# Performance work log

Hardware: AMD Instinct MI355X
Metric: run time of the kernel (lower is better)

The kernel has to match this reference:

```python
import jax, jax.numpy as jnp
import numpy as np


def setup_inputs() -> dict:
    key = jax.random.key(0)
    k1, k2, k3, k4 = jax.random.split(key, 4)
    N, E, D, B = 50000, 100000, 64, 16
    atom_features = jax.random.normal(k1, (N, D), dtype=jnp.float32)
    bond_features = jax.random.normal(k2, (E, B), dtype=jnp.float32)
    pair_indices = jax.random.randint(k3, (E, 2), 0, N, dtype=jnp.int32)
    kernel = jax.random.normal(k4, (B, D * D), dtype=jnp.float32) * (1.0 / np.sqrt(B))
    bias = jnp.zeros((D * D,), dtype=jnp.float32)
    return {
        "atom_features": atom_features,
        "bond_features": bond_features,
        "pair_indices": pair_indices,
        "kernel": kernel,
        "bias": bias,
    }


def reference(atom_features, bond_features, pair_indices, kernel, bias):
    N, D = atom_features.shape
    # Per-edge transformation matrix: [E, D, D]
    edge_mat = (bond_features @ kernel + bias).reshape(-1, D, D)
    # Gather neighbor atom features: [E, D]
    neighbors = atom_features[pair_indices[:, 1]]
    # Per-edge matvec (matmul with expand/squeeze in original): [E, D]
    transformed = jnp.einsum("eij,ej->ei", edge_mat, neighbors)
    # Scatter-add into destination atoms: [N, D]
    aggregated = jax.ops.segment_sum(transformed, pair_indices[:, 0], num_segments=N)
    return aggregated
```

## Files before the change

kernel.cpp:

```cpp
#include <hip/hip_runtime.h>

typedef _Float16 half8  __attribute__((ext_vector_type(8)));
typedef _Float16 half2v __attribute__((ext_vector_type(2)));
typedef float    f32x4  __attribute__((ext_vector_type(4)));

#define BB 16
#define NB_B 17
#define BM 128
#define NT 8
#define PACK_BLKS 34
#define ZERO_BLKS 1024

__device__ __forceinline__ void gll16(const void* g, void* l) {
  __builtin_amdgcn_global_load_lds(
      (const __attribute__((address_space(1))) void*)g,
      (__attribute__((address_space(3))) void*)l, 16, 0, 0);
}

__global__ void prep(const float* __restrict__ kern, const float* __restrict__ bias,
                     _Float16* __restrict__ ktg, f32x4* __restrict__ out4, int n4) {
  if (blockIdx.x < PACK_BLKS) {
    int g = blockIdx.x * 256 + threadIdx.x;
    int s = g >> 8, t = (g >> 6) & 3, l = g & 63;
    int i = t * 16 + (l & 15);
    int k0 = s * 32 + (l >> 4) * 8;
    _Float16 v[8];
#pragma unroll
    for (int e = 0; e < 8; ++e) {
      int k = k0 + e, b = k >> 6, j = k & 63;
      float x = (b < BB) ? kern[b * 4096 + i * 64 + j] : bias[i * 64 + j];
      v[e] = (_Float16)x;
    }
    size_t dst = (size_t)(s >> 1) * 4096 + (size_t)(s & 1) * 2048 + t * 512 + l * 8;
    *(half8*)(ktg + dst) = *(const half8*)v;
  } else {
    int i = (blockIdx.x - PACK_BLKS) * 256 + threadIdx.x;
    for (; i < n4; i += ZERO_BLKS * 256) out4[i] = (f32x4){0.f, 0.f, 0.f, 0.f};
  }
}

__global__ __launch_bounds__(256, 4)
void edge_gemm(const float* __restrict__ atom, const float* __restrict__ bond,
               const int* __restrict__ pair, const _Float16* __restrict__ ktg,
               float* __restrict__ out, int E) {
  __shared__ __align__(16) _Float16 nb[BM * 64];
  __shared__ __align__(16) char bbuf[2][8192];
  __shared__ __align__(16) _Float16 bndh[NB_B * 16 * NT];
  __shared__ int srcs[BM];
  __shared__ int nbrs[BM];

  const int tid = threadIdx.x;
  const int e0  = blockIdx.x * BM;

  if (tid < BM) {
    const int e = e0 + tid;
    const bool valid = e < E;
    int2 p2 = valid ? *(const int2*)(pair + 2 * e) : (int2){0, 0};
    srcs[tid] = p2.x;
    nbrs[tid] = p2.y;
  }
  gll16((const char*)ktg + tid * 16,        (char*)bbuf[0] + tid * 16);
  gll16((const char*)ktg + 4096 + tid * 16, (char*)bbuf[0] + 4096 + tid * 16);
  __syncthreads();

  if (tid < BM) {
    const int e = e0 + tid;
    const bool valid = e < E;
    const int wl = tid & 15, wt = tid >> 4;
    const f32x4* brow = (const f32x4*)(bond + (size_t)e * BB);
#pragma unroll
    for (int q = 0; q < 4; ++q) {
      f32x4 bv = {0.f, 0.f, 0.f, 0.f};
      if (valid) bv = brow[q];
#pragma unroll
      for (int z = 0; z < 4; ++z)
        bndh[((q * 4 + z) * 16 + wl) * NT + wt] = (_Float16)bv[z];
    }
    bndh[(16 * 16 + wl) * NT + wt] = valid ? (_Float16)1.0f : (_Float16)0.0f;
  }

#pragma unroll
  for (int it = 0; it < 4; ++it) {
    const int idx = it * 256 + tid;
    const int r = idx >> 3, c8 = idx & 7;
    const int nbr = nbrs[r];
    const bool valid = (e0 + r) < E;
    f32x4 x0 = {0.f,0.f,0.f,0.f}, x1 = {0.f,0.f,0.f,0.f};
    if (valid) {
      const f32x4* arow = (const f32x4*)(atom + (size_t)nbr * 64);
      x0 = arow[2 * c8]; x1 = arow[2 * c8 + 1];
    }
    _Float16 h[8];
    h[0] = (_Float16)x0[0]; h[1] = (_Float16)x0[1]; h[2] = (_Float16)x0[2]; h[3] = (_Float16)x0[3];
    h[4] = (_Float16)x1[0]; h[5] = (_Float16)x1[1]; h[6] = (_Float16)x1[2]; h[7] = (_Float16)x1[3];
    *(half8*)((char*)nb + r * 128 + ((c8 ^ (r & 7)) << 4)) = *(const half8*)h;
  }
  __syncthreads();

  const int lane = tid & 63, wave = tid >> 6;
  const int l15 = lane & 15, lg = lane >> 4;

  half8 a[NT][2];
#pragma unroll
  for (int t = 0; t < NT; ++t) {
    const int r = t * 16 + l15;
    const int rb = r * 128, sw = (r & 7) << 4;
#pragma unroll
    for (int p = 0; p < 2; ++p)
      a[t][p] = *(const half8*)((const char*)nb + rb + (((p * 4 + lg) << 4) ^ sw));
  }

  f32x4 acc[NT];
#pragma unroll
  for (int t = 0; t < NT; ++t) acc[t] = (f32x4){0.f, 0.f, 0.f, 0.f};

  for (int b = 0; b < NB_B; ++b) {
    if (b + 1 < NB_B) {
      const char* src = (const char*)ktg + (size_t)(b + 1) * 8192;
      char* dst = (char*)bbuf[(b + 1) & 1];
      gll16(src + tid * 16,        dst + tid * 16);
      gll16(src + 4096 + tid * 16, dst + 4096 + tid * 16);
    }
    const half8 sv = *(const half8*)&bndh[(b * 16 + l15) * NT];
    const char* bp = (const char*)bbuf[b & 1] + wave * 1024 + lane * 16;
#pragma unroll
    for (int sp = 0; sp < 2; ++sp) {
      const half8 bf = *(const half8*)(bp + sp * 4096);
#pragma unroll
      for (int t = 0; t < NT; ++t) {
        const _Float16 s = sv[t];
        const half2v sc = {s, s};
        half8 as = a[t][sp];
        half2v* ap = (half2v*)&as;
#pragma unroll
        for (int q = 0; q < 4; ++q) ap[q] = ap[q] * sc;
        acc[t] = __builtin_amdgcn_mfma_f32_16x16x32_f16(as, bf, acc[t], 0, 0, 0);
      }
    }
    __syncthreads();
  }

#pragma unroll
  for (int t = 0; t < NT; ++t) {
#pragma unroll
    for (int rr = 0; rr < 4; ++rr) {
      const int el = t * 16 + lg * 4 + rr;
      if (e0 + el < E)
        atomicAdd(out + (size_t)srcs[el] * 64 + wave * 16 + l15, acc[t][rr]);
    }
  }
}

extern "C" void kernel_launch(void* const* d_in, const int* in_sizes, int n_in,
                              void* d_out, int out_size, void* d_ws, size_t ws_size,
                              hipStream_t stream) {
  const float* atom = (const float*)d_in[0];
  const float* bond = (const float*)d_in[1];
  const int*   pair = (const int*)d_in[2];
  const float* kern = (const float*)d_in[3];
  const float* bias = (const float*)d_in[4];
  float* out = (float*)d_out;
  _Float16* ktg = (_Float16*)d_ws;

  const int E  = in_sizes[1] / BB;
  const int n4 = out_size / 4;

  prep<<<PACK_BLKS + ZERO_BLKS, 256, 0, stream>>>(kern, bias, ktg, (f32x4*)out, n4);
  edge_gemm<<<(E + BM - 1) / BM, 256, 0, stream>>>(atom, bond, pair, ktg, out, E);
}
```

Before: 115.1 us.

## Load kernel tiles directly to registers with 2x2 wave tiling, drop LDS staging

```diff
diff --git a/kernel.cpp b/kernel.cpp
--- a/kernel.cpp
+++ b/kernel.cpp
@@ -1,6 +1,7 @@
 #include <hip/hip_runtime.h>
 
 typedef _Float16 half8  __attribute__((ext_vector_type(8)));
+typedef _Float16 half4v __attribute__((ext_vector_type(4)));
 typedef _Float16 half2v __attribute__((ext_vector_type(2)));
 typedef float    f32x4  __attribute__((ext_vector_type(4)));
 
@@ -10,12 +11,6 @@
 #define NT 8
 #define PACK_BLKS 34
 #define ZERO_BLKS 1024
-
-__device__ __forceinline__ void gll16(const void* g, void* l) {
-  __builtin_amdgcn_global_load_lds(
-      (const __attribute__((address_space(1))) void*)g,
-      (__attribute__((address_space(3))) void*)l, 16, 0, 0);
-}
 
 __global__ void prep(const float* __restrict__ kern, const float* __restrict__ bias,
                      _Float16* __restrict__ ktg, f32x4* __restrict__ out4, int n4) {
@@ -39,12 +34,11 @@
   }
 }
 
-__global__ __launch_bounds__(256, 4)
+__global__ __launch_bounds__(256, 3)
 void edge_gemm(const float* __restrict__ atom, const float* __restrict__ bond,
                const int* __restrict__ pair, const _Float16* __restrict__ ktg,
                float* __restrict__ out, int E) {
   __shared__ __align__(16) _Float16 nb[BM * 64];
-  __shared__ __align__(16) char bbuf[2][8192];
   __shared__ __align__(16) _Float16 bndh[NB_B * 16 * NT];
   __shared__ int srcs[BM];
   __shared__ int nbrs[BM];
@@ -59,8 +53,6 @@
     srcs[tid] = p2.x;
     nbrs[tid] = p2.y;
   }
-  gll16((const char*)ktg + tid * 16,        (char*)bbuf[0] + tid * 16);
-  gll16((const char*)ktg + 4096 + tid * 16, (char*)bbuf[0] + 4096 + tid * 16);
   __syncthreads();
 
   if (tid < BM) {
@@ -98,55 +90,69 @@
   __syncthreads();
 
   const int lane = tid & 63, wave = tid >> 6;
+  const int wm = wave >> 1, wn = wave & 1;
   const int l15 = lane & 15, lg = lane >> 4;
 
-  half8 a[NT][2];
+  half8 a[4][2];
 #pragma unroll
-  for (int t = 0; t < NT; ++t) {
-    const int r = t * 16 + l15;
+  for (int t = 0; t < 4; ++t) {
+    const int r = wm * 64 + t * 16 + l15;
     const int rb = r * 128, sw = (r & 7) << 4;
 #pragma unroll
     for (int p = 0; p < 2; ++p)
       a[t][p] = *(const half8*)((const char*)nb + rb + (((p * 4 + lg) << 4) ^ sw));
   }
 
-  f32x4 acc[NT];
+  f32x4 acc[4][2];
 #pragma unroll
-  for (int t = 0; t < NT; ++t) acc[t] = (f32x4){0.f, 0.f, 0.f, 0.f};
+  for (int t = 0; t < 4; ++t) {
+    acc[t][0] = (f32x4){0.f, 0.f, 0.f, 0.f};
+    acc[t][1] = (f32x4){0.f, 0.f, 0.f, 0.f};
+  }
 
-  for (int b = 0; b < NB_B; ++b) {
-    if (b + 1 < NB_B) {
-      const char* src = (const char*)ktg + (size_t)(b + 1) * 8192;
-      char* dst = (char*)bbuf[(b + 1) & 1];
-      gll16(src + tid * 16,        dst + tid * 16);
-      gll16(src + 4096 + tid * 16, dst + 4096 + tid * 16);
+  const _Float16* bp  = ktg + (size_t)wn * 1024 + (size_t)lane * 8;
+  const _Float16* scp = &bndh[l15 * NT + wm * 4];
+
+  half8 bf[3][4];
+#pragma unroll
+  for (int rr = 0; rr < 3; ++rr)
+#pragma unroll
+    for (int f = 0; f < 4; ++f)
+      bf[rr][f] = *(const half8*)(bp + rr * 4096 + (f >> 1) * 2048 + (f & 1) * 512);
+
+#pragma unroll
+  for (int r = 0; r < NB_B; ++r) {
+    const int slot = r % 3;
+    const half4v sv = *(const half4v*)(scp + r * 128);
+#pragma unroll
+    for (int t = 0; t < 4; ++t) {
+      const half2v sc = {sv[t], sv[t]};
+      half8 a0 = a[t][0], a1 = a[t][1];
+      half2v* a0p = (half2v*)&a0; half2v* a1p = (half2v*)&a1;
+#pragma unroll
+      for (int q = 0; q < 4; ++q) { a0p[q] = a0p[q] * sc; a1p[q] = a1p[q] * sc; }
+      acc[t][0] = __builtin_amdgcn_mfma_f32_16x16x32_f16(a0, bf[slot][0], acc[t][0], 0, 0, 0);
+      acc[t][1] = __builtin_amdgcn_mfma_f32_16x16x32_f16(a0, bf[slot][1], acc[t][1], 0, 0, 0);
+      acc[t][0] = __builtin_amdgcn_mfma_f32_16x16x32_f16(a1, bf[slot][2], acc[t][0], 0, 0, 0);
+      acc[t][1] = __builtin_amdgcn_mfma_f32_16x16x32_f16(a1, bf[slot][3], acc[t][1], 0, 0, 0);
     }
-    const half8 sv = *(const half8*)&bndh[(b * 16 + l15) * NT];
-    const char* bp = (const char*)bbuf[b & 1] + wave * 1024 + lane * 16;
+    if (r + 3 < NB_B) {
 #pragma unroll
-    for (int sp = 0; sp < 2; ++sp) {
-      const half8 bf = *(const half8*)(bp + sp * 4096);
-#pragma unroll
-      for (int t = 0; t < NT; ++t) {
-        const _Float16 s = sv[t];
-        const half2v sc = {s, s};
-        half8 as = a[t][sp];
-        half2v* ap = (half2v*)&as;
-#pragma unroll
-        for (int q = 0; q < 4; ++q) ap[q] = ap[q] * sc;
-        acc[t] = __builtin_amdgcn_mfma_f32_16x16x32_f16(as, bf, acc[t], 0, 0, 0);
-      }
+      for (int f = 0; f < 4; ++f)
+        bf[slot][f] = *(const half8*)(bp + (r + 3) * 4096 + (f >> 1) * 2048 + (f & 1) * 512);
     }
-    __syncthreads();
   }
 
 #pragma unroll
-  for (int t = 0; t < NT; ++t) {
+  for (int t = 0; t < 4; ++t) {
 #pragma unroll
     for (int rr = 0; rr < 4; ++rr) {
-      const int el = t * 16 + lg * 4 + rr;
-      if (e0 + el < E)
-        atomicAdd(out + (size_t)srcs[el] * 64 + wave * 16 + l15, acc[t][rr]);
+      const int el = wm * 64 + t * 16 + lg * 4 + rr;
+      if (e0 + el < E) {
+        float* dst = out + (size_t)srcs[el] * 64 + wn * 32 + l15;
+        atomicAdd(dst,      acc[t][0][rr]);
+        atomicAdd(dst + 16, acc[t][1][rr]);
+      }
     }
   }
 }
```

Result: faster. 110.9 us (-3.6%).

## Halve edge tile to 64 and use a 2x2 wave tiling of MFMA outputs

Applied to the files above, without the earlier changes.

```diff
diff --git a/kernel.cpp b/kernel.cpp
--- a/kernel.cpp
+++ b/kernel.cpp
@@ -6,8 +6,7 @@
 
 #define BB 16
 #define NB_B 17
-#define BM 128
-#define NT 8
+#define BM 64
 #define PACK_BLKS 34
 #define ZERO_BLKS 1024
 
@@ -39,13 +38,13 @@
   }
 }
 
-__global__ __launch_bounds__(256, 4)
+__global__ __launch_bounds__(256, 5)
 void edge_gemm(const float* __restrict__ atom, const float* __restrict__ bond,
                const int* __restrict__ pair, const _Float16* __restrict__ ktg,
                float* __restrict__ out, int E) {
   __shared__ __align__(16) _Float16 nb[BM * 64];
   __shared__ __align__(16) char bbuf[2][8192];
-  __shared__ __align__(16) _Float16 bndh[NB_B * 16 * NT];
+  __shared__ _Float16 bndh[NB_B * BM];
   __shared__ int srcs[BM];
   __shared__ int nbrs[BM];
 
@@ -66,21 +65,19 @@
   if (tid < BM) {
     const int e = e0 + tid;
     const bool valid = e < E;
-    const int wl = tid & 15, wt = tid >> 4;
     const f32x4* brow = (const f32x4*)(bond + (size_t)e * BB);
 #pragma unroll
     for (int q = 0; q < 4; ++q) {
       f32x4 bv = {0.f, 0.f, 0.f, 0.f};
       if (valid) bv = brow[q];
 #pragma unroll
-      for (int z = 0; z < 4; ++z)
-        bndh[((q * 4 + z) * 16 + wl) * NT + wt] = (_Float16)bv[z];
+      for (int z = 0; z < 4; ++z) bndh[(q * 4 + z) * BM + tid] = (_Float16)bv[z];
     }
-    bndh[(16 * 16 + wl) * NT + wt] = valid ? (_Float16)1.0f : (_Float16)0.0f;
+    bndh[16 * BM + tid] = valid ? (_Float16)1.0f : (_Float16)0.0f;
   }
 
 #pragma unroll
-  for (int it = 0; it < 4; ++it) {
+  for (int it = 0; it < 2; ++it) {
     const int idx = it * 256 + tid;
     const int r = idx >> 3, c8 = idx & 7;
     const int nbr = nbrs[r];
@@ -98,21 +95,24 @@
   __syncthreads();
 
   const int lane = tid & 63, wave = tid >> 6;
+  const int wm = wave >> 1, wn = wave & 1;
   const int l15 = lane & 15, lg = lane >> 4;
 
-  half8 a[NT][2];
+  half8 a[2][2];
 #pragma unroll
-  for (int t = 0; t < NT; ++t) {
-    const int r = t * 16 + l15;
+  for (int t = 0; t < 2; ++t) {
+    const int r = wm * 32 + t * 16 + l15;
     const int rb = r * 128, sw = (r & 7) << 4;
 #pragma unroll
     for (int p = 0; p < 2; ++p)
       a[t][p] = *(const half8*)((const char*)nb + rb + (((p * 4 + lg) << 4) ^ sw));
   }
 
-  f32x4 acc[NT];
+  f32x4 acc[2][2];
 #pragma unroll
-  for (int t = 0; t < NT; ++t) acc[t] = (f32x4){0.f, 0.f, 0.f, 0.f};
+  for (int t = 0; t < 2; ++t)
+#pragma unroll
+    for (int n = 0; n < 2; ++n) acc[t][n] = (f32x4){0.f, 0.f, 0.f, 0.f};
 
   for (int b = 0; b < NB_B; ++b) {
     if (b + 1 < NB_B) {
@@ -121,32 +121,36 @@
       gll16(src + tid * 16,        dst + tid * 16);
       gll16(src + 4096 + tid * 16, dst + 4096 + tid * 16);
     }
-    const half8 sv = *(const half8*)&bndh[(b * 16 + l15) * NT];
-    const char* bp = (const char*)bbuf[b & 1] + wave * 1024 + lane * 16;
+    const _Float16 s0 = bndh[b * BM + wm * 32 + l15];
+    const _Float16 s1 = bndh[b * BM + wm * 32 + 16 + l15];
+    const half2v sc0 = {s0, s0}, sc1 = {s1, s1};
+    const char* bp = (const char*)bbuf[b & 1] + (size_t)(wn * 2) * 1024 + lane * 16;
 #pragma unroll
     for (int sp = 0; sp < 2; ++sp) {
-      const half8 bf = *(const half8*)(bp + sp * 4096);
+      half8 a0 = a[0][sp], a1 = a[1][sp];
+      half2v* a0p = (half2v*)&a0; half2v* a1p = (half2v*)&a1;
 #pragma unroll
-      for (int t = 0; t < NT; ++t) {
-        const _Float16 s = sv[t];
-        const half2v sc = {s, s};
-        half8 as = a[t][sp];
-        half2v* ap = (half2v*)&as;
+      for (int q = 0; q < 4; ++q) { a0p[q] = a0p[q] * sc0; a1p[q] = a1p[q] * sc1; }
 #pragma unroll
-        for (int q = 0; q < 4; ++q) ap[q] = ap[q] * sc;
-        acc[t] = __builtin_amdgcn_mfma_f32_16x16x32_f16(as, bf, acc[t], 0, 0, 0);
+      for (int nt = 0; nt < 2; ++nt) {
+        const half8 bf = *(const half8*)(bp + sp * 4096 + nt * 1024);
+        acc[0][nt] = __builtin_amdgcn_mfma_f32_16x16x32_f16(a0, bf, acc[0][nt], 0, 0, 0);
+        acc[1][nt] = __builtin_amdgcn_mfma_f32_16x16x32_f16(a1, bf, acc[1][nt], 0, 0, 0);
       }
     }
     __syncthreads();
   }
 
 #pragma unroll
-  for (int t = 0; t < NT; ++t) {
+  for (int t = 0; t < 2; ++t) {
 #pragma unroll
     for (int rr = 0; rr < 4; ++rr) {
-      const int el = t * 16 + lg * 4 + rr;
-      if (e0 + el < E)
-        atomicAdd(out + (size_t)srcs[el] * 64 + wave * 16 + l15, acc[t][rr]);
+      const int el = wm * 32 + t * 16 + lg * 4 + rr;
+      if (e0 + el < E) {
+        float* dst = out + (size_t)srcs[el] * 64 + wn * 32 + l15;
+        atomicAdd(dst,      acc[t][0][rr]);
+        atomicAdd(dst + 16, acc[t][1][rr]);
+      }
     }
   }
 }
```

New measurement: 109.1 us. 1.05x faster.
